# Performance work log

Measured on AMD Instinct MI355X. Metric: run time of the kernel, lower is better.

The kernel has to match this reference:

```python
import jax, jax.numpy as jnp
import numpy as np

B, H, N = 2, 4, 4096


def setup_inputs() -> dict:
    key = jax.random.key(0)
    ranking = jax.random.normal(key, (B, H, N, 1), dtype=jnp.float32)
    return {"ranking": ranking}


def reference(ranking):
    b_s, h, n = ranking.shape[:3]
    r = ranking[..., 0]  # [b, h, n]
    # stable descending argsort of ranking*100 (negate; jnp stable sort keeps tie order)
    sorted_idx = jnp.argsort(-r * 100.0, axis=2, stable=True)  # [b, h, n] int
    r_sort = jnp.take_along_axis(r, sorted_idx, axis=2)
    # rel_scaler = cumsum of ones = 1..n (no mask case)
    rel_scaler = jnp.cumsum(jnp.ones_like(r_sort), axis=2)
    rel_minus = jnp.cumsum(r_sort, axis=2)
    relative_ranking = rel_minus - rel_scaler * r_sort
    rel_scaler = jnp.maximum(rel_scaler - 1.0, 0.0)  # 0..n-1
    # Hrelu forward: hard ReLU (custom backward in torch; forward math is relu)
    rank = jax.nn.relu(relative_ranking)
    indicator = rel_scaler - rank
    indicator = jnp.where(indicator < 0, indicator + n, indicator)
    perm_value = jnp.exp(-indicator * 10.0)
    # sparse COO (bh, row, col) -> coalesce == scatter-add into dense [b*h, n, n]
    rows = rel_scaler.astype(jnp.int32).reshape(b_s * h, n)
    cols = sorted_idx.reshape(b_s * h, n).astype(jnp.int32)
    vals = perm_value.reshape(b_s * h, n)
    bh = jnp.arange(b_s * h, dtype=jnp.int32)[:, None]
    perm = jnp.zeros((b_s * h, n, n), jnp.float32).at[bh, rows, cols].add(vals)
    return perm
```

## Files before the change

kernel.cpp:

```cpp
#include <hip/hip_runtime.h>
#include <math.h>
#include <float.h>

#define N 4096
#define BH 8
#define THREADS 256
#define PARTS 32
#define EPB 128
#define EPT 4
#define SLICES 8
#define KPS (N / SLICES)
#define CHUNK (N / THREADS)

__device__ __forceinline__ unsigned long long desc_key64(float r, int i) {
    float k = r * 100.0f;
    unsigned int b = __float_as_uint(k);
    unsigned int asc = (b & 0x80000000u) ? ~b : (b | 0x80000000u);
    return ((unsigned long long)(~asc) << 32) | (unsigned int)i;
}

__global__ __launch_bounds__(THREADS)
void rank_kernel(const float* __restrict__ ranking,
                 int* __restrict__ cols,
                 float* __restrict__ rsort) {
    __shared__ unsigned long long keys[N];
    __shared__ unsigned short partial[SLICES * EPB];

    const int bh   = blockIdx.x / PARTS;
    const int part = blockIdx.x % PARTS;
    const float* r = ranking + (size_t)bh * N;

    for (int i = threadIdx.x; i < N; i += THREADS)
        keys[i] = desc_key64(r[i], i);
    __syncthreads();

    const int g = threadIdx.x & 31;
    const int s = threadIdx.x >> 5;
    const int e_base = g * EPT;

    unsigned long long mykey[EPT];
    #pragma unroll
    for (int j = 0; j < EPT; ++j)
        mykey[j] = keys[part * EPB + e_base + j];

    int cnt0 = 0, cnt1 = 0, cnt2 = 0, cnt3 = 0;
    const ulonglong2* k2 = (const ulonglong2*)(keys + s * KPS);
    #pragma unroll 4
    for (int k = 0; k < KPS / 2; ++k) {
        ulonglong2 kk = k2[k];
        cnt0 += (kk.x < mykey[0]) + (kk.y < mykey[0]);
        cnt1 += (kk.x < mykey[1]) + (kk.y < mykey[1]);
        cnt2 += (kk.x < mykey[2]) + (kk.y < mykey[2]);
        cnt3 += (kk.x < mykey[3]) + (kk.y < mykey[3]);
    }
    partial[s * EPB + e_base + 0] = (unsigned short)cnt0;
    partial[s * EPB + e_base + 1] = (unsigned short)cnt1;
    partial[s * EPB + e_base + 2] = (unsigned short)cnt2;
    partial[s * EPB + e_base + 3] = (unsigned short)cnt3;
    __syncthreads();

    if (threadIdx.x < EPB) {
        int rank = 0;
        #pragma unroll
        for (int t = 0; t < SLICES; ++t)
            rank += (int)partial[t * EPB + threadIdx.x];
        int e = part * EPB + threadIdx.x;
        size_t o = (size_t)bh * N + rank;
        cols[o]  = e;
        rsort[o] = r[e];
    }
}

__global__ __launch_bounds__(THREADS)
void scan_kernel(const float* __restrict__ rsort,
                 float* __restrict__ vals) {
    __shared__ double chunk_sums[THREADS];

    const int bh  = blockIdx.x;
    const int tid = threadIdx.x;
    const float* rs = rsort + (size_t)bh * N;
    const int base = tid * CHUNK;

    float  v[CHUNK];
    double local[CHUNK];
    const float4* f4 = (const float4*)(rs + base);
    #pragma unroll
    for (int q = 0; q < CHUNK / 4; ++q) {
        float4 w = f4[q];
        v[q * 4 + 0] = w.x; v[q * 4 + 1] = w.y;
        v[q * 4 + 2] = w.z; v[q * 4 + 3] = w.w;
    }
    double s = 0.0;
    #pragma unroll
    for (int q = 0; q < CHUNK; ++q) { s += (double)v[q]; local[q] = s; }
    chunk_sums[tid] = s;
    __syncthreads();

    double off = 0.0;
    for (int t = 0; t < tid; ++t) off += chunk_sums[t];

    #pragma unroll
    for (int q = 0; q < CHUNK; ++q) {
        int i = base + q;
        double cumsum = off + local[q];
        double rel    = cumsum - (double)(i + 1) * (double)v[q];
        double rank   = rel > 0.0 ? rel : 0.0;
        double ind    = (double)i - rank;
        if (ind < 0.0) ind += (double)N;
        if (ind < 0.0) ind = 0.0;
        vals[(size_t)bh * N + i] = (float)exp(ind * -10.0);
    }
}

__global__ __launch_bounds__(THREADS)
void fill_kernel(const int* __restrict__ cols,
                 const float* __restrict__ vals,
                 float* __restrict__ out) {
    const size_t row = blockIdx.x;
    const int   c = cols[row];
    const float v = vals[row];
    float4* o = (float4*)(out + row * (size_t)N);
    const int fc  = c >> 2;
    const int tid = threadIdx.x;
    #pragma unroll
    for (int q = 0; q < 4; ++q) {
        int f = tid + THREADS * q;
        float4 w = {0.f, 0.f, 0.f, 0.f};
        if (f == fc) ((float*)&w)[c & 3] = v;
        o[f] = w;
    }
}

extern "C" void kernel_launch(void* const* d_in, const int* in_sizes, int n_in,
                              void* d_out, int out_size, void* d_ws, size_t ws_size,
                              hipStream_t stream) {
    const float* ranking = (const float*)d_in[0];
    float* out = (float*)d_out;

    int*   cols  = (int*)d_ws;
    float* rsort = (float*)((char*)d_ws + sizeof(int)   * (size_t)BH * N);
    float* vals  = (float*)((char*)d_ws + sizeof(int)*2 * (size_t)BH * N);

    rank_kernel<<<BH * PARTS, THREADS, 0, stream>>>(ranking, cols, rsort);
    scan_kernel<<<BH, THREADS, 0, stream>>>(rsort, vals);
    fill_kernel<<<BH * N, THREADS, 0, stream>>>(cols, vals, out);
}
```

Baseline: 556.4 us.

## Fuse rank and scan via last-block counter, batch fill rows per block

Merges the rank and scan kernels into one launch: each block increments a per-bh atomic counter after writing its ranks, and the last block to finish runs the prefix-scan for that bh. The fill kernel now launches 2048 blocks that each write 16 rows instead of one block per row, and key construction loads ranking with float4. This removes one kernel launch and reduces block scheduling overhead for the large zero-fill, at the cost of an extra memset launch, threadfence synchronisation, and a serialized scan tail inside one block per bh.

```diff
diff --git a/kernel.cpp b/kernel.cpp
--- a/kernel.cpp
+++ b/kernel.cpp
@@ -1,6 +1,5 @@
 #include <hip/hip_runtime.h>
 #include <math.h>
-#include <float.h>
 
 #define N 4096
 #define BH 8
@@ -11,6 +10,8 @@
 #define SLICES 8
 #define KPS (N / SLICES)
 #define CHUNK (N / THREADS)
+#define FILL_BLOCKS 2048
+#define ROWS_PER_BLOCK (BH * N / FILL_BLOCKS)
 
 __device__ __forceinline__ unsigned long long desc_key64(float r, int i) {
     float k = r * 100.0f;
@@ -20,18 +21,28 @@
 }
 
 __global__ __launch_bounds__(THREADS)
-void rank_kernel(const float* __restrict__ ranking,
-                 int* __restrict__ cols,
-                 float* __restrict__ rsort) {
+void rank_scan_kernel(const float* __restrict__ ranking,
+                      int* __restrict__ cols,
+                      float* __restrict__ rsort,
+                      float* __restrict__ vals,
+                      unsigned int* __restrict__ counters) {
     __shared__ unsigned long long keys[N];
     __shared__ unsigned short partial[SLICES * EPB];
+    __shared__ double chunk_sums[THREADS];
+    __shared__ int lds_is_last;
 
     const int bh   = blockIdx.x / PARTS;
     const int part = blockIdx.x % PARTS;
     const float* r = ranking + (size_t)bh * N;
 
-    for (int i = threadIdx.x; i < N; i += THREADS)
-        keys[i] = desc_key64(r[i], i);
+    const float4* r4 = (const float4*)r;
+    for (int i = threadIdx.x; i < N / 4; i += THREADS) {
+        float4 w = r4[i];
+        keys[i * 4 + 0] = desc_key64(w.x, i * 4 + 0);
+        keys[i * 4 + 1] = desc_key64(w.y, i * 4 + 1);
+        keys[i * 4 + 2] = desc_key64(w.z, i * 4 + 2);
+        keys[i * 4 + 3] = desc_key64(w.w, i * 4 + 3);
+    }
     __syncthreads();
 
     const int g = threadIdx.x & 31;
@@ -69,18 +80,19 @@
         cols[o]  = e;
         rsort[o] = r[e];
     }
-}
 
-__global__ __launch_bounds__(THREADS)
-void scan_kernel(const float* __restrict__ rsort,
-                 float* __restrict__ vals) {
-    __shared__ double chunk_sums[THREADS];
+    __threadfence();
+    __syncthreads();
+    if (threadIdx.x == 0) {
+        unsigned int old = atomicAdd(&counters[bh], 1u);
+        lds_is_last = (old == PARTS - 1) ? 1 : 0;
+    }
+    __syncthreads();
+    if (!lds_is_last) return;
+    __threadfence();
 
-    const int bh  = blockIdx.x;
-    const int tid = threadIdx.x;
     const float* rs = rsort + (size_t)bh * N;
-    const int base = tid * CHUNK;
-
+    const int base = threadIdx.x * CHUNK;
     float  v[CHUNK];
     double local[CHUNK];
     const float4* f4 = (const float4*)(rs + base);
@@ -90,14 +102,14 @@
         v[q * 4 + 0] = w.x; v[q * 4 + 1] = w.y;
         v[q * 4 + 2] = w.z; v[q * 4 + 3] = w.w;
     }
-    double s = 0.0;
+    double ssum = 0.0;
     #pragma unroll
-    for (int q = 0; q < CHUNK; ++q) { s += (double)v[q]; local[q] = s; }
-    chunk_sums[tid] = s;
+    for (int q = 0; q < CHUNK; ++q) { ssum += (double)v[q]; local[q] = ssum; }
+    chunk_sums[threadIdx.x] = ssum;
     __syncthreads();
 
     double off = 0.0;
-    for (int t = 0; t < tid; ++t) off += chunk_sums[t];
+    for (int t = 0; t < threadIdx.x; ++t) off += chunk_sums[t];
 
     #pragma unroll
     for (int q = 0; q < CHUNK; ++q) {
@@ -116,18 +128,21 @@
 void fill_kernel(const int* __restrict__ cols,
                  const float* __restrict__ vals,
                  float* __restrict__ out) {
-    const size_t row = blockIdx.x;
-    const int   c = cols[row];
-    const float v = vals[row];
-    float4* o = (float4*)(out + row * (size_t)N);
-    const int fc  = c >> 2;
     const int tid = threadIdx.x;
-    #pragma unroll
-    for (int q = 0; q < 4; ++q) {
-        int f = tid + THREADS * q;
-        float4 w = {0.f, 0.f, 0.f, 0.f};
-        if (f == fc) ((float*)&w)[c & 3] = v;
-        o[f] = w;
+    const size_t row0 = (size_t)blockIdx.x * ROWS_PER_BLOCK;
+    for (int rr = 0; rr < ROWS_PER_BLOCK; ++rr) {
+        const size_t row = row0 + rr;
+        const int   c = cols[row];
+        const float v = vals[row];
+        float4* o = (float4*)(out + row * (size_t)N);
+        const int fc = c >> 2;
+        #pragma unroll
+        for (int q = 0; q < 4; ++q) {
+            int f = tid + THREADS * q;
+            float4 w = {0.f, 0.f, 0.f, 0.f};
+            if (f == fc) ((float*)&w)[c & 3] = v;
+            o[f] = w;
+        }
     }
 }
 
@@ -138,10 +153,11 @@
     float* out = (float*)d_out;
 
     int*   cols  = (int*)d_ws;
-    float* rsort = (float*)((char*)d_ws + sizeof(int)   * (size_t)BH * N);
-    float* vals  = (float*)((char*)d_ws + sizeof(int)*2 * (size_t)BH * N);
+    float* rsort = (float*)((char*)d_ws + sizeof(int)     * (size_t)BH * N);
+    float* vals  = (float*)((char*)d_ws + sizeof(int) * 2 * (size_t)BH * N);
+    unsigned int* counters = (unsigned int*)((char*)d_ws + sizeof(int) * 3 * (size_t)BH * N);
 
-    rank_kernel<<<BH * PARTS, THREADS, 0, stream>>>(ranking, cols, rsort);
-    scan_kernel<<<BH, THREADS, 0, stream>>>(rsort, vals);
-    fill_kernel<<<BH * N, THREADS, 0, stream>>>(cols, vals, out);
+    hipMemsetAsync(counters, 0, BH * sizeof(unsigned int), stream);
+    rank_scan_kernel<<<BH * PARTS, THREADS, 0, stream>>>(ranking, cols, rsort, vals, counters);
+    fill_kernel<<<FILL_BLOCKS, THREADS, 0, stream>>>(cols, vals, out);
 }
```

After: 587.7 us. 5.6% more time.
